# Kernel tuning notes

Measured on AMD Instinct MI355X. Metric: run time of the kernel, lower is better.

Reference implementation:

```python
import jax, jax.numpy as jnp
import numpy as np


def setup_inputs() -> dict:
    key = jax.random.key(0)
    B, C, L = 32, 512, 4096
    inputs = jax.random.normal(key, (B, C, L), dtype=jnp.float32)
    return {"inputs": inputs, "top_k": 8}


def reference(inputs, top_k):
    # inputs: [B, C, L]. Select top_k values along last dim, keep original order.
    _, top_idxs = jax.lax.top_k(inputs, top_k)          # [B, C, k] indices of k largest
    sorted_idxs = jnp.sort(top_idxs, axis=2)            # restore positional order
    return jnp.take_along_axis(inputs, sorted_idxs, axis=2)  # [B, C, k]
```

## Files before the change

### kernel.cpp

```cpp
#include <hip/hip_runtime.h>
#include <cstdint>
#include <math.h>

#define ROW_LEN 4096
#define KSEL 8
#define NT 256
#define EPT 16

__device__ inline unsigned umaxu(unsigned a, unsigned b) { return a > b ? a : b; }
__device__ inline unsigned uminu(unsigned a, unsigned b) { return a > b ? b : a; }
__device__ inline unsigned ordkey(float f) {
    int t = __float_as_int(f);
    return (unsigned)(t ^ ((t >> 31) | 0x80000000));
}
__device__ inline float unkey(unsigned u) {
    int t = (int)u;
    return __int_as_float(t < 0 ? (t ^ 0x80000000) : ~t);
}

__global__ __launch_bounds__(NT) void kmax_kernel(const float* __restrict__ in,
                                                  float* __restrict__ out) {
    const int row  = blockIdx.x;
    const int tid  = threadIdx.x;
    const int lane = tid & 63;
    const int wave = tid >> 6;

    const float4* p4 = reinterpret_cast<const float4*>(in + (size_t)row * ROW_LEN + (size_t)tid * EPT);

    unsigned k[EPT];
#pragma unroll
    for (int j = 0; j < 4; ++j) {
        float4 a = p4[j];
        k[j * 4 + 0] = ordkey(a.x);
        k[j * 4 + 1] = ordkey(a.y);
        k[j * 4 + 2] = ordkey(a.z);
        k[j * 4 + 3] = ordkey(a.w);
    }

    unsigned t[EPT];
#pragma unroll
    for (int s = 0; s < EPT; ++s) t[s] = k[s];

#define CED(i, j) { unsigned a_ = t[i], b_ = t[j]; t[i] = umaxu(a_, b_); t[j] = uminu(a_, b_); }
#define SORT8D(o) \
    CED(o+0,o+1) CED(o+2,o+3) CED(o+4,o+5) CED(o+6,o+7) \
    CED(o+0,o+2) CED(o+1,o+3) CED(o+4,o+6) CED(o+5,o+7) \
    CED(o+1,o+2) CED(o+5,o+6) \
    CED(o+0,o+4) CED(o+1,o+5) CED(o+2,o+6) CED(o+3,o+7) \
    CED(o+2,o+4) CED(o+3,o+5) \
    CED(o+1,o+2) CED(o+3,o+4) CED(o+5,o+6)

    SORT8D(0)
    SORT8D(8)
#pragma unroll
    for (int s = 0; s < 8; ++s) t[s] = umaxu(t[s], t[15 - s]);
    CED(0,4) CED(1,5) CED(2,6) CED(3,7)
    CED(0,2) CED(1,3) CED(4,6) CED(5,7)
    CED(0,1) CED(2,3) CED(4,5) CED(6,7)

    __shared__ unsigned sred[KSEL][4];
    __shared__ unsigned swsum[4];

    unsigned Tkey = 0;
#pragma unroll
    for (int it = 0; it < KSEL; ++it) {
        unsigned h = t[0];
        unsigned m = h;
#pragma unroll
        for (int off = 32; off > 0; off >>= 1)
            m = umaxu(m, (unsigned)__shfl_xor((int)m, off, 64));
        if (lane == 0) sred[it][wave] = m;
        __syncthreads();
        unsigned m0 = sred[it][0], m1 = sred[it][1], m2 = sred[it][2], m3 = sred[it][3];
        unsigned M = umaxu(umaxu(m0, m1), umaxu(m2, m3));
        int wsel = (m0 == M) ? 0 : (m1 == M) ? 1 : (m2 == M) ? 2 : 3;
        bool cand = (wave == wsel) && (h == M);
        unsigned long long b = __ballot(cand);
        bool amFirst = cand && ((b & ((1ull << lane) - 1)) == 0ull);
        if (amFirst) {
            t[0] = t[1]; t[1] = t[2]; t[2] = t[3]; t[3] = t[4];
            t[4] = t[5]; t[5] = t[6]; t[6] = t[7]; t[7] = 0u;
        }
        Tkey = M;
    }

    int cgt = 0, ceq = 0;
#pragma unroll
    for (int s = 0; s < EPT; ++s) {
        cgt += (k[s] > Tkey);
        ceq += (k[s] == Tkey);
    }
    unsigned packed = ((unsigned)cgt << 16) | (unsigned)ceq;
    unsigned p = packed;
#pragma unroll
    for (int off = 1; off < 64; off <<= 1) {
        unsigned o = (unsigned)__shfl_up((int)p, off, 64);
        if (lane >= off) p += o;
    }
    if (lane == 63) swsum[wave] = p;
    __syncthreads();
    unsigned basep = 0, total = 0;
#pragma unroll
    for (int w = 0; w < 4; ++w) {
        unsigned ws = swsum[w];
        total += ws;
        if (w < wave) basep += ws;
    }
    unsigned excl = basep + p - packed;
    int totgt = (int)(total >> 16), toteq = (int)(total & 0xFFFFu);
    int pgt = (int)(excl >> 16), peq = (int)(excl & 0xFFFFu);
    int Q = KSEL - totgt;
    int mybase = pgt + (peq < Q ? peq : Q);
    float* op = out + (size_t)row * KSEL + mybase;

    if (totgt + toteq == KSEL) {
#pragma unroll
        for (int s = 0; s < EPT; ++s) {
            if (k[s] >= Tkey) { *op++ = unkey(k[s]); }
        }
    } else {
        int myq = Q - peq; myq = myq < 0 ? 0 : myq;
        int eqSeen = 0;
#pragma unroll
        for (int s = 0; s < EPT; ++s) {
            bool iseq = (k[s] == Tkey);
            bool sel = (k[s] > Tkey) || (iseq && (eqSeen < myq));
            eqSeen += iseq;
            if (sel) { *op++ = unkey(k[s]); }
        }
    }
}

extern "C" void kernel_launch(void* const* d_in, const int* in_sizes, int n_in,
                              void* d_out, int out_size, void* d_ws, size_t ws_size,
                              hipStream_t stream) {
    const float* in  = (const float*)d_in[0];
    float*       out = (float*)d_out;
    const int rows = in_sizes[0] / ROW_LEN;
    kmax_kernel<<<rows, NT, 0, stream>>>(in, out);
}
```

Baseline: 355.4 us.

## Replace iterative k-pass max extraction with butterfly top-8 merge on floats

```diff
diff --git a/kernel.cpp b/kernel.cpp
--- a/kernel.cpp
+++ b/kernel.cpp
@@ -1,22 +1,25 @@
 #include <hip/hip_runtime.h>
 #include <cstdint>
-#include <math.h>
 
 #define ROW_LEN 4096
 #define KSEL 8
 #define NT 256
 #define EPT 16
 
-__device__ inline unsigned umaxu(unsigned a, unsigned b) { return a > b ? a : b; }
-__device__ inline unsigned uminu(unsigned a, unsigned b) { return a > b ? b : a; }
-__device__ inline unsigned ordkey(float f) {
-    int t = __float_as_int(f);
-    return (unsigned)(t ^ ((t >> 31) | 0x80000000));
-}
-__device__ inline float unkey(unsigned u) {
-    int t = (int)u;
-    return __int_as_float(t < 0 ? (t ^ 0x80000000) : ~t);
-}
+#define CEDA(a, i, j) { float x_ = a[i], y_ = a[j]; a[i] = fmaxf(x_, y_); a[j] = fminf(x_, y_); }
+
+#define SORT8D(a, o) \
+    CEDA(a,o+0,o+1) CEDA(a,o+2,o+3) CEDA(a,o+4,o+5) CEDA(a,o+6,o+7) \
+    CEDA(a,o+0,o+2) CEDA(a,o+1,o+3) CEDA(a,o+4,o+6) CEDA(a,o+5,o+7) \
+    CEDA(a,o+1,o+2) CEDA(a,o+5,o+6) \
+    CEDA(a,o+0,o+4) CEDA(a,o+1,o+5) CEDA(a,o+2,o+6) CEDA(a,o+3,o+7) \
+    CEDA(a,o+2,o+4) CEDA(a,o+3,o+5) \
+    CEDA(a,o+1,o+2) CEDA(a,o+3,o+4) CEDA(a,o+5,o+6)
+
+#define BMERGE8D(a) \
+    CEDA(a,0,4) CEDA(a,1,5) CEDA(a,2,6) CEDA(a,3,7) \
+    CEDA(a,0,2) CEDA(a,1,3) CEDA(a,4,6) CEDA(a,5,7) \
+    CEDA(a,0,1) CEDA(a,2,3) CEDA(a,4,5) CEDA(a,6,7)
 
 __global__ __launch_bounds__(NT) void kmax_kernel(const float* __restrict__ in,
                                                   float* __restrict__ out) {
@@ -27,68 +30,61 @@
 
     const float4* p4 = reinterpret_cast<const float4*>(in + (size_t)row * ROW_LEN + (size_t)tid * EPT);
 
-    unsigned k[EPT];
+    float k[EPT];
 #pragma unroll
     for (int j = 0; j < 4; ++j) {
         float4 a = p4[j];
-        k[j * 4 + 0] = ordkey(a.x);
-        k[j * 4 + 1] = ordkey(a.y);
-        k[j * 4 + 2] = ordkey(a.z);
-        k[j * 4 + 3] = ordkey(a.w);
+        k[j * 4 + 0] = a.x;
+        k[j * 4 + 1] = a.y;
+        k[j * 4 + 2] = a.z;
+        k[j * 4 + 3] = a.w;
     }
 
-    unsigned t[EPT];
+    float t[EPT];
 #pragma unroll
     for (int s = 0; s < EPT; ++s) t[s] = k[s];
+    SORT8D(t, 0)
+    SORT8D(t, 8)
+#pragma unroll
+    for (int s = 0; s < 8; ++s) t[s] = fmaxf(t[s], t[15 - s]);
+    BMERGE8D(t)
 
-#define CED(i, j) { unsigned a_ = t[i], b_ = t[j]; t[i] = umaxu(a_, b_); t[j] = uminu(a_, b_); }
-#define SORT8D(o) \
-    CED(o+0,o+1) CED(o+2,o+3) CED(o+4,o+5) CED(o+6,o+7) \
-    CED(o+0,o+2) CED(o+1,o+3) CED(o+4,o+6) CED(o+5,o+7) \
-    CED(o+1,o+2) CED(o+5,o+6) \
-    CED(o+0,o+4) CED(o+1,o+5) CED(o+2,o+6) CED(o+3,o+7) \
-    CED(o+2,o+4) CED(o+3,o+5) \
-    CED(o+1,o+2) CED(o+3,o+4) CED(o+5,o+6)
+#pragma unroll
+    for (int off = 1; off < 64; off <<= 1) {
+        float o[8];
+#pragma unroll
+        for (int s = 0; s < 8; ++s) o[s] = __shfl_xor(t[s], off, 64);
+#pragma unroll
+        for (int s = 0; s < 8; ++s) t[s] = fmaxf(t[s], o[7 - s]);
+        BMERGE8D(t)
+    }
 
-    SORT8D(0)
-    SORT8D(8)
-#pragma unroll
-    for (int s = 0; s < 8; ++s) t[s] = umaxu(t[s], t[15 - s]);
-    CED(0,4) CED(1,5) CED(2,6) CED(3,7)
-    CED(0,2) CED(1,3) CED(4,6) CED(5,7)
-    CED(0,1) CED(2,3) CED(4,5) CED(6,7)
-
-    __shared__ unsigned sred[KSEL][4];
+    __shared__ float    W[4][KSEL];
     __shared__ unsigned swsum[4];
 
-    unsigned Tkey = 0;
+    if (lane == 0) {
+        float4* wp = reinterpret_cast<float4*>(&W[wave][0]);
+        wp[0] = make_float4(t[0], t[1], t[2], t[3]);
+        wp[1] = make_float4(t[4], t[5], t[6], t[7]);
+    }
+    __syncthreads();
+
+    float A[8], B[8];
 #pragma unroll
-    for (int it = 0; it < KSEL; ++it) {
-        unsigned h = t[0];
-        unsigned m = h;
+    for (int s = 0; s < 8; ++s) A[s] = fmaxf(W[0][s], W[1][7 - s]);
+    BMERGE8D(A)
 #pragma unroll
-        for (int off = 32; off > 0; off >>= 1)
-            m = umaxu(m, (unsigned)__shfl_xor((int)m, off, 64));
-        if (lane == 0) sred[it][wave] = m;
-        __syncthreads();
-        unsigned m0 = sred[it][0], m1 = sred[it][1], m2 = sred[it][2], m3 = sred[it][3];
-        unsigned M = umaxu(umaxu(m0, m1), umaxu(m2, m3));
-        int wsel = (m0 == M) ? 0 : (m1 == M) ? 1 : (m2 == M) ? 2 : 3;
-        bool cand = (wave == wsel) && (h == M);
-        unsigned long long b = __ballot(cand);
-        bool amFirst = cand && ((b & ((1ull << lane) - 1)) == 0ull);
-        if (amFirst) {
-            t[0] = t[1]; t[1] = t[2]; t[2] = t[3]; t[3] = t[4];
-            t[4] = t[5]; t[5] = t[6]; t[6] = t[7]; t[7] = 0u;
-        }
-        Tkey = M;
-    }
+    for (int s = 0; s < 8; ++s) B[s] = fmaxf(W[2][s], W[3][7 - s]);
+    BMERGE8D(B)
+    float T = fmaxf(A[0], B[7]);
+#pragma unroll
+    for (int s = 1; s < 8; ++s) T = fminf(T, fmaxf(A[s], B[7 - s]));
 
     int cgt = 0, ceq = 0;
 #pragma unroll
     for (int s = 0; s < EPT; ++s) {
-        cgt += (k[s] > Tkey);
-        ceq += (k[s] == Tkey);
+        cgt += (k[s] > T);
+        ceq += (k[s] == T);
     }
     unsigned packed = ((unsigned)cgt << 16) | (unsigned)ceq;
     unsigned p = packed;
@@ -106,27 +102,27 @@
         total += ws;
         if (w < wave) basep += ws;
     }
-    unsigned excl = basep + p - packed;
+    unsigned excl  = basep + p - packed;
     int totgt = (int)(total >> 16), toteq = (int)(total & 0xFFFFu);
-    int pgt = (int)(excl >> 16), peq = (int)(excl & 0xFFFFu);
-    int Q = KSEL - totgt;
+    int pgt   = (int)(excl  >> 16), peq   = (int)(excl  & 0xFFFFu);
+    int Q      = KSEL - totgt;
     int mybase = pgt + (peq < Q ? peq : Q);
-    float* op = out + (size_t)row * KSEL + mybase;
+    float* op  = out + (size_t)row * KSEL + mybase;
 
     if (totgt + toteq == KSEL) {
 #pragma unroll
         for (int s = 0; s < EPT; ++s) {
-            if (k[s] >= Tkey) { *op++ = unkey(k[s]); }
+            if (k[s] >= T) { *op++ = k[s]; }
         }
     } else {
         int myq = Q - peq; myq = myq < 0 ? 0 : myq;
         int eqSeen = 0;
 #pragma unroll
         for (int s = 0; s < EPT; ++s) {
-            bool iseq = (k[s] == Tkey);
-            bool sel = (k[s] > Tkey) || (iseq && (eqSeen < myq));
+            bool iseq = (k[s] == T);
+            bool sel  = (k[s] > T) || (iseq && (eqSeen < myq));
             eqSeen += iseq;
-            if (sel) { *op++ = unkey(k[s]); }
+            if (sel) { *op++ = k[s]; }
         }
     }
 }
```

Measured after the change: 361.2 us. No clear change (+1.6%).
